# Performance work log

Measured on AMD Instinct MI355X. Metric: run time of the kernel, lower is better.

## Reference

```python
import jax, jax.numpy as jnp
import numpy as np

D_MODEL = 1024
NUM_HEADS = 16
HEAD_DIM = D_MODEL // NUM_HEADS


def setup_inputs() -> dict:
    key = jax.random.key(0)
    ks = jax.random.split(key, 5)
    B, S, D_IN = 2, 2048, 1024
    x = jax.random.normal(ks[0], (B, S, D_IN), dtype=jnp.float32)
    std = 0.02
    wq = jax.random.normal(ks[1], (D_MODEL, D_IN), dtype=jnp.float32) * std
    wk = jax.random.normal(ks[2], (D_MODEL, D_IN), dtype=jnp.float32) * std
    wv = jax.random.normal(ks[3], (D_MODEL, D_IN), dtype=jnp.float32) * std
    wo = jax.random.normal(ks[4], (D_IN, D_MODEL), dtype=jnp.float32) * std
    return {"x": x, "wq": wq, "wk": wk, "wv": wv, "wo": wo}


def _mha(x, wq, wk, wv, wo):
    B, S, _ = x.shape
    H, Dh = NUM_HEADS, HEAD_DIM
    # projections: Linear applies x @ W.T with W of shape [out, in]
    q = (x @ wq.T).reshape(B, S, H, Dh).transpose(0, 2, 1, 3)  # [B,H,S,Dh]
    k = (x @ wk.T).reshape(B, S, H, Dh).transpose(0, 2, 1, 3)
    v = (x @ wv.T).reshape(B, S, H, Dh).transpose(0, 2, 1, 3)
    scores = jnp.einsum('bhqd,bhkd->bhqk', q, k) / jnp.sqrt(jnp.float32(Dh))
    causal = jnp.tril(jnp.ones((S, S), dtype=bool))  # True where attended
    scores = jnp.where(causal, scores, -jnp.inf)
    attn = jax.nn.softmax(scores, axis=-1)
    out = jnp.einsum('bhqk,bhkd->bhqd', attn, v)  # [B,H,S,Dh]
    out = out.transpose(0, 2, 1, 3).reshape(B, S, H * Dh)
    return out @ wo.T


def reference(x, wq, wk, wv, wo):
    return _mha(x, wq, wk, wv, wo)
```

## Files before the change

### kernel.cpp

```cpp
#include <hip/hip_runtime.h>
#include <hip/hip_bf16.h>
#include <stdint.h>

using bf16 = __hip_bfloat16;
typedef __attribute__((ext_vector_type(4))) short shorts4;
typedef __attribute__((ext_vector_type(8))) short short8;
typedef __attribute__((ext_vector_type(4))) float floatx4;
typedef __attribute__((ext_vector_type(16))) float floatx16;
typedef __attribute__((ext_vector_type(4))) unsigned int uintx4;

constexpr int BATCH = 2;
constexpr int SEQ   = 2048;
constexpr int NH    = 16;
constexpr int DH    = 64;
constexpr int DM    = 1024;
constexpr int MROWS = BATCH * SEQ;
constexpr int OUTN  = MROWS * DM;
constexpr int WN    = DM * DM;

__device__ inline short bfbits(float x) {
    bf16 h = __float2bfloat16(x);
    return __builtin_bit_cast(short, h);
}

__device__ inline unsigned pack2(float a, float b) {
    return (unsigned)(unsigned short)bfbits(a) |
           ((unsigned)(unsigned short)bfbits(b) << 16);
}

__device__ inline void async16(bf16* lds, const bf16* g) {
    __builtin_amdgcn_global_load_lds(
        (const __attribute__((address_space(1))) unsigned int*)g,
        (__attribute__((address_space(3))) unsigned int*)lds, 16, 0, 0);
}

__device__ inline void cvt8(const float* src, bf16* dst) {
    float4 f0 = *(const float4*)(src);
    float4 f1 = *(const float4*)(src + 4);
    short8 o;
    o[0] = bfbits(f0.x); o[1] = bfbits(f0.y); o[2] = bfbits(f0.z); o[3] = bfbits(f0.w);
    o[4] = bfbits(f1.x); o[5] = bfbits(f1.y); o[6] = bfbits(f1.z); o[7] = bfbits(f1.w);
    *(short8*)(dst) = o;
}

__global__ __launch_bounds__(256)
void cvt_all(const float* __restrict__ x,  const float* __restrict__ wq,
             const float* __restrict__ wk, const float* __restrict__ wv,
             const float* __restrict__ wo, bf16* __restrict__ dst,
             bf16* __restrict__ wob)
{
    const size_t i = ((size_t)blockIdx.x * 256 + threadIdx.x) * 8;
    if (i < (size_t)OUTN + 3 * WN) {
        const float* src; size_t off;
        if (i < (size_t)OUTN)               { src = x;  off = i; }
        else if (i < (size_t)OUTN + WN)     { src = wq; off = i - OUTN; }
        else if (i < (size_t)OUTN + 2 * WN) { src = wk; off = i - OUTN - WN; }
        else                                { src = wv; off = i - OUTN - 2 * (size_t)WN; }
        cvt8(src + off, dst + i);
    } else {
        const size_t off = i - OUTN - 3 * (size_t)WN;
        cvt8(wo + off, wob + off);
    }
}

__global__ __launch_bounds__(256)
void cvt_inputs(const float* __restrict__ x,  const float* __restrict__ wq,
                const float* __restrict__ wk, const float* __restrict__ wv,
                bf16* __restrict__ dst)
{
    const size_t i = ((size_t)blockIdx.x * 256 + threadIdx.x) * 8;
    const float* src; size_t off;
    if (i < (size_t)OUTN)               { src = x;  off = i; }
    else if (i < (size_t)OUTN + WN)     { src = wq; off = i - OUTN; }
    else if (i < (size_t)OUTN + 2 * WN) { src = wk; off = i - OUTN - WN; }
    else                                { src = wv; off = i - OUTN - 2 * (size_t)WN; }
    cvt8(src + off, dst + i);
}

__global__ __launch_bounds__(256)
void cvt_wo(const float* __restrict__ wo, bf16* __restrict__ dst)
{
    const size_t i = ((size_t)blockIdx.x * 256 + threadIdx.x) * 8;
    cvt8(wo + i, dst + i);
}

template<int MODE, int NZ>
__global__ __launch_bounds__(512, 2)
void gemm_mfma(const bf16* __restrict__ A,
               const bf16* __restrict__ W0, const bf16* __restrict__ W1,
               const bf16* __restrict__ W2,
               bf16* __restrict__ C0, bf16* __restrict__ C1, bf16* __restrict__ C2,
               float* __restrict__ F)
{
    __shared__ __align__(16) bf16 smem[(1 + NZ) * 8192 * 2];

    const int t    = threadIdx.x;
    const int wave = t >> 6;
    const int lane = t & 63;
    const int quad = lane >> 4;
    const int l16  = lane & 15;
    const int m0 = blockIdx.y * 128;
    const int n0 = blockIdx.x * 128;
    const int wr = (wave >> 2) * 64;
    const int wc = (wave & 3) * 32;

    const bf16* Wp[3] = {W0, W1, W2};

    floatx4 acc[NZ][4][2] = {};

    auto stage = [&](int kt, int bb) {
        bf16* Bb = smem + bb * (1 + NZ) * 8192;
        const int k0 = kt * 64;
        #pragma unroll
        for (int p = 0; p < 2; p++) {
            const int ck = p * 512 + t;
            const int kr = ck >> 3;
            const int kg = (ck & 7) ^ (kr & 7);
            async16(Bb + ck * 8, A + (size_t)(m0 + kr) * DM + k0 + kg * 8);
            #pragma unroll
            for (int zz = 0; zz < NZ; zz++)
                async16(Bb + (1 + zz) * 8192 + ck * 8,
                        Wp[zz] + (size_t)(n0 + kr) * DM + k0 + kg * 8);
        }
    };

    stage(0, 0);
    __syncthreads();

    for (int kt = 0; kt < DM / 64; ++kt) {
        const int cur = kt & 1;
        if (kt + 1 < DM / 64) stage(kt + 1, cur ^ 1);

        const bf16* Bb = smem + cur * (1 + NZ) * 8192;

        #pragma unroll
        for (int ks = 0; ks < 2; ks++) {
            short8 af[4];
            #pragma unroll
            for (int i = 0; i < 4; i++) {
                const int r = wr + i * 16 + l16;
                af[i] = *(const short8*)(Bb + r * 64 + ((ks * 4 + quad) ^ (r & 7)) * 8);
            }
            #pragma unroll
            for (int zz = 0; zz < NZ; zz++) {
                short8 wf[2];
                #pragma unroll
                for (int j = 0; j < 2; j++) {
                    const int n = wc + j * 16 + l16;
                    wf[j] = *(const short8*)(Bb + (1 + zz) * 8192 + n * 64 +
                                             ((ks * 4 + quad) ^ (n & 7)) * 8);
                }
                __builtin_amdgcn_s_setprio(1);
                #pragma unroll
                for (int i = 0; i < 4; i++)
                    #pragma unroll
                    for (int j = 0; j < 2; j++)
                        acc[zz][i][j] = __builtin_amdgcn_mfma_f32_16x16x32_bf16(
                            af[i], wf[j], acc[zz][i][j], 0, 0, 0);
                __builtin_amdgcn_s_setprio(0);
            }
        }
        __syncthreads();
    }

    #pragma unroll
    for (int zz = 0; zz < NZ; zz++) {
        #pragma unroll
        for (int i = 0; i < 4; i++) {
            #pragma unroll
            for (int j = 0; j < 2; j++) {
                if (MODE == 0 && zz == 2) {
                    const int s0 = m0 + wr + i * 16 + quad * 4;
                    const int gn = n0 + wc + j * 16 + l16;
                    const int b = s0 >> 11, sr = s0 & (SEQ - 1);
                    const int h = gn >> 6,  d = gn & (DH - 1);
                    shorts4 pv;
                    #pragma unroll
                    for (int r = 0; r < 4; r++) pv[r] = bfbits(acc[zz][i][j][r]);
                    *(shorts4*)(C2 + (((size_t)(b * NH + h)) * DH + d) * SEQ + sr) = pv;
                } else {
                    #pragma unroll
                    for (int r = 0; r < 4; r++) {
                        const int gm = m0 + wr + i * 16 + quad * 4 + r;
                        const int gn = n0 + wc + j * 16 + l16;
                        if (MODE == 1) {
                            F[(size_t)gm * DM + gn] = acc[zz][i][j][r];
                        } else {
                            float av = acc[zz][i][j][r];
                            if (zz == 0) av *= 0.18033688f;
                            bf16* dst = (zz == 0) ? C0 : C1;
                            dst[(size_t)gm * DM + gn] = __float2bfloat16(av);
                        }
                    }
                }
            }
        }
    }
}

__global__ __launch_bounds__(512, 4)
void attn_flash(bf16* __restrict__ Q, const bf16* __restrict__ K,
                const bf16* __restrict__ Vt)
{
    __shared__ __align__(16) bf16 smem[32768];

    const int t    = threadIdx.x;
    const int wave = t >> 6;
    const int lane = t & 63;
    const int hi   = lane >> 5;
    const int l32  = lane & 31;

    const int h  = blockIdx.y;
    const int b  = blockIdx.z;
    const int qt = (blockIdx.x + 5 * h + 8 * b) & 15;
    const int q0 = qt * 128;
    const int hc = h * DH;
    const size_t rowb = (size_t)b * SEQ;
    const size_t bhv  = ((size_t)(b * NH + h)) * SEQ * DH;

    const int qw    = wave & 3;
    const int khalf = wave >> 2;
    const int qrow  = q0 + qw * 32;
    const int qg    = qrow + l32;

    short8 qf[4];
    #pragma unroll
    for (int s = 0; s < 4; s++)
        qf[s] = *(const short8*)(Q + (rowb + qg) * DM + hc + s * 16 + hi * 8);

    floatx16 oacc[2] = {};
    float lsum = 0.f;

    const int T = q0 / 128 + 1;

    auto stage = [&](int tt, int bb) {
        bf16* Kb = smem + bb * 16384;
        bf16* Vb = Kb + 8192;
        const int k0 = tt * 128;
        #pragma unroll
        for (int p = 0; p < 2; p++) {
            const int ck = p * 512 + t;
            const int kr = ck >> 3;
            const int kg = (ck & 7) ^ (kr & 7);
            async16(Kb + ck * 8, K + (rowb + k0 + kr) * DM + hc + kg * 8);
            const int vr = ck >> 4;
            const int vg = (ck & 15) ^ (vr & 15);
            async16(Vb + ck * 8, Vt + bhv + (size_t)vr * SEQ + k0 + vg * 8);
        }
    };

    stage(0, 0);
    __syncthreads();

    for (int tt = 0; tt < T; ++tt) {
        const int cur = tt & 1;
        if (tt + 1 < T) stage(tt + 1, cur ^ 1);

        const bf16* Ks = smem + cur * 16384;
        const bf16* Vs = Ks + 8192;
        const int kbase = tt * 128 + khalf * 64;

        if (kbase <= qrow + 31) {
            #pragma unroll
            for (int kt = 0; kt < 2; kt++) {
                const int kb = kbase + kt * 32;
                if (kb > qrow + 31) continue;

                const int krow = khalf * 64 + kt * 32 + l32;
                floatx16 sc = {};
                #pragma unroll
                for (int s = 0; s < 4; s++) {
                    const int g = (s * 2 + hi) ^ (krow & 7);
                    short8 kf = *(const short8*)(Ks + krow * 64 + g * 8);
                    sc = __builtin_amdgcn_mfma_f32_32x32x16_bf16(kf, qf[s], sc, 0, 0, 0);
                }

                if (kb + 31 > qrow) {
                    #pragma unroll
                    for (int r = 0; r < 16; r++) {
                        const int key = kb + (r & 3) + 8 * (r >> 2) + 4 * hi;
                        sc[r] = (key <= qg) ? sc[r] : -1e30f;
                    }
                }

                #pragma unroll
                for (int r = 0; r < 16; r++) {
                    const float p = __builtin_amdgcn_exp2f(sc[r]);
                    sc[r] = p;
                    lsum += p;
                }

                unsigned d[4][2];
                #pragma unroll
                for (int g = 0; g < 4; g++) {
                    d[g][0] = pack2(sc[4 * g + 0], sc[4 * g + 1]);
                    d[g][1] = pack2(sc[4 * g + 2], sc[4 * g + 3]);
                }

                #pragma unroll
                for (int h16 = 0; h16 < 2; h16++) {
                    const unsigned a0 = d[h16 * 2][0],     a1 = d[h16 * 2][1];
                    const unsigned b0 = d[h16 * 2 + 1][0], b1 = d[h16 * 2 + 1][1];
                    const unsigned mine0 = hi ? b0 : a0, mine1 = hi ? b1 : a1;
                    const unsigned give0 = hi ? a0 : b0, give1 = hi ? a1 : b1;
                    const unsigned r0 = (unsigned)__shfl_xor((int)give0, 32, 64);
                    const unsigned r1 = (unsigned)__shfl_xor((int)give1, 32, 64);
                    uintx4 pw;
                    pw[0] = hi ? r0 : mine0;
                    pw[1] = hi ? r1 : mine1;
                    pw[2] = hi ? mine0 : r0;
                    pw[3] = hi ? mine1 : r1;
                    short8 pb = __builtin_bit_cast(short8, pw);

                    const int Gbase = khalf * 8 + kt * 4 + h16 * 2 + hi;
                    #pragma unroll
                    for (int tile = 0; tile < 2; tile++) {
                        const int vrow = tile * 32 + l32;
                        const int vg = Gbase ^ (vrow & 15);
                        short8 vf = *(const short8*)(Vs + vrow * 128 + vg * 8);
                        oacc[tile] = __builtin_amdgcn_mfma_f32_32x32x16_bf16(vf, pb, oacc[tile], 0, 0, 0);
                    }
                }
            }
        }
        __syncthreads();
    }

    lsum += __shfl_xor(lsum, 32, 64);

    float* dmp = (float*)smem;
    float* lP  = dmp + 4 * 32 * 65;
    if (wave >= 4) {
        const int p = wave - 4;
        #pragma unroll
        for (int tile = 0; tile < 2; tile++)
            #pragma unroll
            for (int r = 0; r < 16; r++) {
                const int d = tile * 32 + (r & 3) + 8 * (r >> 2) + 4 * hi;
                dmp[(p * 32 + l32) * 65 + d] = oacc[tile][r];
            }
        if (!hi) lP[p * 32 + l32] = lsum;
    }
    __syncthreads();

    if (wave < 4) {
        const int p = wave;
        lsum += lP[p * 32 + l32];
        const float invl = 1.0f / lsum;

        bf16* T8 = smem + 16896 + wave * (32 * 72);
        #pragma unroll
        for (int tile = 0; tile < 2; tile++)
            #pragma unroll
            for (int rq = 0; rq < 4; rq++) {
                shorts4 v4;
                #pragma unroll
                for (int s = 0; s < 4; s++) {
                    const int r = rq * 4 + s;
                    const int d = tile * 32 + (r & 3) + 8 * (r >> 2) + 4 * hi;
                    const float comb = oacc[tile][r] + dmp[(p * 32 + l32) * 65 + d];
                    v4[s] = bfbits(comb * invl);
                }
                *(shorts4*)(T8 + l32 * 72 + tile * 32 + rq * 8 + hi * 4) = v4;
            }
        asm volatile("s_waitcnt lgkmcnt(0)" ::: "memory");
        #pragma unroll
        for (int p2 = 0; p2 < 4; p2++) {
            const int rq = (lane >> 3) + p2 * 8;
            const int dd = (lane & 7) * 8;
            short8 v8 = *(const short8*)(T8 + rq * 72 + dd);
            *(short8*)(Q + (rowb + qrow + rq) * DM + hc + dd) = v8;
        }
    }
}

extern "C" void kernel_launch(void* const* d_in, const int* in_sizes, int n_in,
                              void* d_out, int out_size, void* d_ws, size_t ws_size,
                              hipStream_t stream)
{
    const float* x  = (const float*)d_in[0];
    const float* wq = (const float*)d_in[1];
    const float* wk = (const float*)d_in[2];
    const float* wv = (const float*)d_in[3];
    const float* wo = (const float*)d_in[4];
    float* out = (float*)d_out;

    bf16* qb = (bf16*)d_ws;
    bf16* kb = qb + (size_t)OUTN;
    bf16* vb = kb + (size_t)OUTN;

    bf16* xb  = (bf16*)d_out;
    bf16* wqb = xb + (size_t)OUTN;
    bf16* wkb = wqb + WN;
    bf16* wvb = wkb + WN;

    const bool wsBig = ws_size >= (size_t)(3 * (size_t)OUTN + WN) * sizeof(bf16);

    if (wsBig) {
        bf16* wob = vb + (size_t)OUTN;
        cvt_all<<<(OUTN + 4 * WN) / (8 * 256), 256, 0, stream>>>(
            x, wq, wk, wv, wo, xb, wob);
        gemm_mfma<0, 3><<<dim3(DM / 128, MROWS / 128), dim3(512), 0, stream>>>(
            xb, wqb, wkb, wvb, qb, kb, vb, nullptr);
        attn_flash<<<dim3(SEQ / 128, NH, BATCH), dim3(512), 0, stream>>>(qb, kb, vb);
        gemm_mfma<1, 1><<<dim3(DM / 128, MROWS / 128), dim3(512), 0, stream>>>(
            qb, wob, nullptr, nullptr, nullptr, nullptr, nullptr, out);
    } else {
        cvt_inputs<<<(OUTN + 3 * WN) / (8 * 256), 256, 0, stream>>>(x, wq, wk, wv, xb);
        gemm_mfma<0, 3><<<dim3(DM / 128, MROWS / 128), dim3(512), 0, stream>>>(
            xb, wqb, wkb, wvb, qb, kb, vb, nullptr);
        attn_flash<<<dim3(SEQ / 128, NH, BATCH), dim3(512), 0, stream>>>(qb, kb, vb);
        bf16* wob = kb;
        cvt_wo<<<WN / (8 * 256), 256, 0, stream>>>(wo, wob);
        gemm_mfma<1, 1><<<dim3(DM / 128, MROWS / 128), dim3(512), 0, stream>>>(
            qb, wob, nullptr, nullptr, nullptr, nullptr, nullptr, out);
    }
}
```

Before: 161.3 us.

## Pair complementary causal query tiles per block with triple-buffered K/V pipeline

Each attention block now handles two query tiles, qt and 15-qt, so every block processes the same 17 key tiles and the causal workload is balanced across blocks. The grid is halved. K/V staging moves from a double buffer to a triple buffer with explicit vmcnt waits and raw barriers, so loads run two stages ahead. In exchange, register pressure rises from holding two sets of Q fragments and accumulators, and LDS per block grows, with launch bounds lowered from 4 to 2 to match.

```diff
diff --git a/kernel.cpp b/kernel.cpp
--- a/kernel.cpp
+++ b/kernel.cpp
@@ -198,11 +198,11 @@
     }
 }
 
-__global__ __launch_bounds__(512, 4)
+__global__ __launch_bounds__(512, 2)
 void attn_flash(bf16* __restrict__ Q, const bf16* __restrict__ K,
                 const bf16* __restrict__ Vt)
 {
-    __shared__ __align__(16) bf16 smem[32768];
+    __shared__ __align__(16) bf16 smem[49152];
 
     const int t    = threadIdx.x;
     const int wave = t >> 6;
@@ -210,33 +210,37 @@
     const int hi   = lane >> 5;
     const int l32  = lane & 31;
 
-    const int h  = blockIdx.y;
-    const int b  = blockIdx.z;
-    const int qt = (blockIdx.x + 5 * h + 8 * b) & 15;
-    const int q0 = qt * 128;
-    const int hc = h * DH;
+    const int h   = blockIdx.y;
+    const int b   = blockIdx.z;
+    const int qtA = blockIdx.x;
+    const int qtB = 15 - qtA;
+    const int hc  = h * DH;
     const size_t rowb = (size_t)b * SEQ;
     const size_t bhv  = ((size_t)(b * NH + h)) * SEQ * DH;
 
     const int qw    = wave & 3;
     const int khalf = wave >> 2;
-    const int qrow  = q0 + qw * 32;
-    const int qg    = qrow + l32;
-
-    short8 qf[4];
+    const int qrA = qtA * 128 + qw * 32;
+    const int qrB = qtB * 128 + qw * 32;
+
+    short8 qfA[4], qfB[4];
     #pragma unroll
-    for (int s = 0; s < 4; s++)
-        qf[s] = *(const short8*)(Q + (rowb + qg) * DM + hc + s * 16 + hi * 8);
-
-    floatx16 oacc[2] = {};
-    float lsum = 0.f;
-
-    const int T = q0 / 128 + 1;
-
-    auto stage = [&](int tt, int bb) {
-        bf16* Kb = smem + bb * 16384;
+    for (int sg = 0; sg < 4; sg++) {
+        qfA[sg] = *(const short8*)(Q + (rowb + qrA + l32) * DM + hc + sg * 16 + hi * 8);
+        qfB[sg] = *(const short8*)(Q + (rowb + qrB + l32) * DM + hc + sg * 16 + hi * 8);
+    }
+
+    floatx16 oaccA[2] = {}, oaccB[2] = {};
+    float lsumA = 0.f, lsumB = 0.f;
+
+    constexpr int NSLOT = 17;
+
+    auto slotK0 = [&](int s) { return (s <= qtA ? s : s - qtA - 1) * 128; };
+
+    auto stage = [&](int s) {
+        bf16* Kb = smem + (s % 3) * 16384;
         bf16* Vb = Kb + 8192;
-        const int k0 = tt * 128;
+        const int k0 = slotK0(s);
         #pragma unroll
         for (int p = 0; p < 2; p++) {
             const int ck = p * 512 + t;
@@ -249,127 +253,143 @@
         }
     };
 
-    stage(0, 0);
+    auto computeStage = [&](int s, int k0, int qrow, const short8* qf,
+                            floatx16* oacc, float& lsum) {
+        const int kbase = k0 + khalf * 64;
+        if (kbase > qrow + 31) return;
+        const bf16* Ks = smem + (s % 3) * 16384;
+        const bf16* Vs = Ks + 8192;
+        const int qg = qrow + l32;
+
+        #pragma unroll
+        for (int kt = 0; kt < 2; kt++) {
+            const int kb = kbase + kt * 32;
+            if (kb > qrow + 31) continue;
+
+            const int krow = khalf * 64 + kt * 32 + l32;
+            floatx16 sc = {};
+            #pragma unroll
+            for (int sg = 0; sg < 4; sg++) {
+                const int g = (sg * 2 + hi) ^ (krow & 7);
+                short8 kf = *(const short8*)(Ks + krow * 64 + g * 8);
+                sc = __builtin_amdgcn_mfma_f32_32x32x16_bf16(kf, qf[sg], sc, 0, 0, 0);
+            }
+
+            if (kb + 31 > qrow) {
+                #pragma unroll
+                for (int r = 0; r < 16; r++) {
+                    const int key = kb + (r & 3) + 8 * (r >> 2) + 4 * hi;
+                    sc[r] = (key <= qg) ? sc[r] : -1e30f;
+                }
+            }
+
+            #pragma unroll
+            for (int r = 0; r < 16; r++) {
+                const float p = __builtin_amdgcn_exp2f(sc[r]);
+                sc[r] = p;
+                lsum += p;
+            }
+
+            unsigned d[4][2];
+            #pragma unroll
+            for (int g = 0; g < 4; g++) {
+                d[g][0] = pack2(sc[4 * g + 0], sc[4 * g + 1]);
+                d[g][1] = pack2(sc[4 * g + 2], sc[4 * g + 3]);
+            }
+
+            #pragma unroll
+            for (int h16 = 0; h16 < 2; h16++) {
+                const unsigned a0 = d[h16 * 2][0],     a1 = d[h16 * 2][1];
+                const unsigned b0 = d[h16 * 2 + 1][0], b1 = d[h16 * 2 + 1][1];
+                const unsigned mine0 = hi ? b0 : a0, mine1 = hi ? b1 : a1;
+                const unsigned give0 = hi ? a0 : b0, give1 = hi ? a1 : b1;
+                const unsigned r0 = (unsigned)__shfl_xor((int)give0, 32, 64);
+                const unsigned r1 = (unsigned)__shfl_xor((int)give1, 32, 64);
+                uintx4 pw;
+                pw[0] = hi ? r0 : mine0;
+                pw[1] = hi ? r1 : mine1;
+                pw[2] = hi ? mine0 : r0;
+                pw[3] = hi ? mine1 : r1;
+                short8 pb = __builtin_bit_cast(short8, pw);
+
+                const int Gbase = khalf * 8 + kt * 4 + h16 * 2 + hi;
+                #pragma unroll
+                for (int tile = 0; tile < 2; tile++) {
+                    const int vrow = tile * 32 + l32;
+                    const int vg = Gbase ^ (vrow & 15);
+                    short8 vf = *(const short8*)(Vs + vrow * 128 + vg * 8);
+                    oacc[tile] = __builtin_amdgcn_mfma_f32_32x32x16_bf16(vf, pb, oacc[tile], 0, 0, 0);
+                }
+            }
+        }
+    };
+
+    stage(0);
+    stage(1);
+    for (int s = 0; s < NSLOT - 1; ++s) {
+        asm volatile("s_waitcnt vmcnt(4)" ::: "memory");
+        __builtin_amdgcn_s_barrier();
+        if (s + 2 < NSLOT) stage(s + 2);
+        if (s <= qtA) computeStage(s, s * 128, qrA, qfA, oaccA, lsumA);
+        else          computeStage(s, (s - qtA - 1) * 128, qrB, qfB, oaccB, lsumB);
+    }
+    asm volatile("s_waitcnt vmcnt(0)" ::: "memory");
+    __builtin_amdgcn_s_barrier();
+    computeStage(NSLOT - 1, (NSLOT - 1 - qtA - 1) * 128, qrB, qfB, oaccB, lsumB);
+
+    lsumA += __shfl_xor(lsumA, 32, 64);
+    lsumB += __shfl_xor(lsumB, 32, 64);
+
     __syncthreads();
-
-    for (int tt = 0; tt < T; ++tt) {
-        const int cur = tt & 1;
-        if (tt + 1 < T) stage(tt + 1, cur ^ 1);
-
-        const bf16* Ks = smem + cur * 16384;
-        const bf16* Vs = Ks + 8192;
-        const int kbase = tt * 128 + khalf * 64;
-
-        if (kbase <= qrow + 31) {
-            #pragma unroll
-            for (int kt = 0; kt < 2; kt++) {
-                const int kb = kbase + kt * 32;
-                if (kb > qrow + 31) continue;
-
-                const int krow = khalf * 64 + kt * 32 + l32;
-                floatx16 sc = {};
-                #pragma unroll
-                for (int s = 0; s < 4; s++) {
-                    const int g = (s * 2 + hi) ^ (krow & 7);
-                    short8 kf = *(const short8*)(Ks + krow * 64 + g * 8);
-                    sc = __builtin_amdgcn_mfma_f32_32x32x16_bf16(kf, qf[s], sc, 0, 0, 0);
-                }
-
-                if (kb + 31 > qrow) {
+    float* dmp = (float*)smem;
+    float* lP  = dmp + 2 * 4 * 32 * 66;
+    if (khalf == 1) {
+        #pragma unroll
+        for (int m = 0; m < 2; m++) {
+            const floatx16* oc = m ? oaccB : oaccA;
+            #pragma unroll
+            for (int tile = 0; tile < 2; tile++)
+                #pragma unroll
+                for (int r = 0; r < 16; r++) {
+                    const int dd = tile * 32 + (r & 3) + 8 * (r >> 2) + 4 * hi;
+                    dmp[((m * 4 + qw) * 32 + l32) * 66 + dd] = oc[tile][r];
+                }
+            if (!hi) lP[(m * 4 + qw) * 32 + l32] = m ? lsumB : lsumA;
+        }
+    }
+    __syncthreads();
+
+    if (khalf == 0) {
+        bf16* T8 = smem + 34304 + qw * 2304;
+        #pragma unroll
+        for (int m = 0; m < 2; m++) {
+            const floatx16* oc = m ? oaccB : oaccA;
+            const float lt = (m ? lsumB : lsumA) + lP[(m * 4 + qw) * 32 + l32];
+            const float invl = 1.0f / lt;
+            const int qrow = m ? qrB : qrA;
+            #pragma unroll
+            for (int tile = 0; tile < 2; tile++)
+                #pragma unroll
+                for (int rq = 0; rq < 4; rq++) {
+                    shorts4 v4;
                     #pragma unroll
-                    for (int r = 0; r < 16; r++) {
-                        const int key = kb + (r & 3) + 8 * (r >> 2) + 4 * hi;
-                        sc[r] = (key <= qg) ? sc[r] : -1e30f;
+                    for (int sg = 0; sg < 4; sg++) {
+                        const int r = rq * 4 + sg;
+                        const int dd = tile * 32 + (r & 3) + 8 * (r >> 2) + 4 * hi;
+                        const float comb = oc[tile][r] + dmp[((m * 4 + qw) * 32 + l32) * 66 + dd];
+                        v4[sg] = bfbits(comb * invl);
                     }
-                }
-
-                #pragma unroll
-                for (int r = 0; r < 16; r++) {
-                    const float p = __builtin_amdgcn_exp2f(sc[r]);
-                    sc[r] = p;
-                    lsum += p;
-                }
-
-                unsigned d[4][2];
-                #pragma unroll
-                for (int g = 0; g < 4; g++) {
-                    d[g][0] = pack2(sc[4 * g + 0], sc[4 * g + 1]);
-                    d[g][1] = pack2(sc[4 * g + 2], sc[4 * g + 3]);
-                }
-
-                #pragma unroll
-                for (int h16 = 0; h16 < 2; h16++) {
-                    const unsigned a0 = d[h16 * 2][0],     a1 = d[h16 * 2][1];
-                    const unsigned b0 = d[h16 * 2 + 1][0], b1 = d[h16 * 2 + 1][1];
-                    const unsigned mine0 = hi ? b0 : a0, mine1 = hi ? b1 : a1;
-                    const unsigned give0 = hi ? a0 : b0, give1 = hi ? a1 : b1;
-                    const unsigned r0 = (unsigned)__shfl_xor((int)give0, 32, 64);
-                    const unsigned r1 = (unsigned)__shfl_xor((int)give1, 32, 64);
-                    uintx4 pw;
-                    pw[0] = hi ? r0 : mine0;
-                    pw[1] = hi ? r1 : mine1;
-                    pw[2] = hi ? mine0 : r0;
-                    pw[3] = hi ? mine1 : r1;
-                    short8 pb = __builtin_bit_cast(short8, pw);
-
-                    const int Gbase = khalf * 8 + kt * 4 + h16 * 2 + hi;
-                    #pragma unroll
-                    for (int tile = 0; tile < 2; tile++) {
-                        const int vrow = tile * 32 + l32;
-                        const int vg = Gbase ^ (vrow & 15);
-                        short8 vf = *(const short8*)(Vs + vrow * 128 + vg * 8);
-                        oacc[tile] = __builtin_amdgcn_mfma_f32_32x32x16_bf16(vf, pb, oacc[tile], 0, 0, 0);
-                    }
-                }
-            }
-        }
-        __syncthreads();
-    }
-
-    lsum += __shfl_xor(lsum, 32, 64);
-
-    float* dmp = (float*)smem;
-    float* lP  = dmp + 4 * 32 * 65;
-    if (wave >= 4) {
-        const int p = wave - 4;
-        #pragma unroll
-        for (int tile = 0; tile < 2; tile++)
-            #pragma unroll
-            for (int r = 0; r < 16; r++) {
-                const int d = tile * 32 + (r & 3) + 8 * (r >> 2) + 4 * hi;
-                dmp[(p * 32 + l32) * 65 + d] = oacc[tile][r];
-            }
-        if (!hi) lP[p * 32 + l32] = lsum;
-    }
-    __syncthreads();
-
-    if (wave < 4) {
-        const int p = wave;
-        lsum += lP[p * 32 + l32];
-        const float invl = 1.0f / lsum;
-
-        bf16* T8 = smem + 16896 + wave * (32 * 72);
-        #pragma unroll
-        for (int tile = 0; tile < 2; tile++)
-            #pragma unroll
-            for (int rq = 0; rq < 4; rq++) {
-                shorts4 v4;
-                #pragma unroll
-                for (int s = 0; s < 4; s++) {
-                    const int r = rq * 4 + s;
-                    const int d = tile * 32 + (r & 3) + 8 * (r >> 2) + 4 * hi;
-                    const float comb = oacc[tile][r] + dmp[(p * 32 + l32) * 65 + d];
-                    v4[s] = bfbits(comb * invl);
-                }
-                *(shorts4*)(T8 + l32 * 72 + tile * 32 + rq * 8 + hi * 4) = v4;
-            }
-        asm volatile("s_waitcnt lgkmcnt(0)" ::: "memory");
-        #pragma unroll
-        for (int p2 = 0; p2 < 4; p2++) {
-            const int rq = (lane >> 3) + p2 * 8;
-            const int dd = (lane & 7) * 8;
-            short8 v8 = *(const short8*)(T8 + rq * 72 + dd);
-            *(short8*)(Q + (rowb + qrow + rq) * DM + hc + dd) = v8;
+                    *(shorts4*)(T8 + l32 * 72 + tile * 32 + rq * 8 + hi * 4) = v4;
+                }
+            asm volatile("s_waitcnt lgkmcnt(0)" ::: "memory");
+            #pragma unroll
+            for (int p2 = 0; p2 < 4; p2++) {
+                const int rq = (lane >> 3) + p2 * 8;
+                const int dd = (lane & 7) * 8;
+                short8 v8 = *(const short8*)(T8 + rq * 72 + dd);
+                *(short8*)(Q + (rowb + qrow + rq) * DM + hc + dd) = v8;
+            }
+            asm volatile("s_waitcnt lgkmcnt(0)" ::: "memory");
         }
     }
 }
@@ -402,14 +422,14 @@
             x, wq, wk, wv, wo, xb, wob);
         gemm_mfma<0, 3><<<dim3(DM / 128, MROWS / 128), dim3(512), 0, stream>>>(
             xb, wqb, wkb, wvb, qb, kb, vb, nullptr);
-        attn_flash<<<dim3(SEQ / 128, NH, BATCH), dim3(512), 0, stream>>>(qb, kb, vb);
+        attn_flash<<<dim3(8, NH, BATCH), dim3(512), 0, stream>>>(qb, kb, vb);
         gemm_mfma<1, 1><<<dim3(DM / 128, MROWS / 128), dim3(512), 0, stream>>>(
             qb, wob, nullptr, nullptr, nullptr, nullptr, nullptr, out);
     } else {
         cvt_inputs<<<(OUTN + 3 * WN) / (8 * 256), 256, 0, stream>>>(x, wq, wk, wv, xb);
         gemm_mfma<0, 3><<<dim3(DM / 128, MROWS / 128), dim3(512), 0, stream>>>(
             xb, wqb, wkb, wvb, qb, kb, vb, nullptr);
-        attn_flash<<<dim3(SEQ / 128, NH, BATCH), dim3(512), 0, stream>>>(qb, kb, vb);
+        attn_flash<<<dim3(8, NH, BATCH), dim3(512), 0, stream>>>(qb, kb, vb);
         bf16* wob = kb;
         cvt_wo<<<WN / (8 * 256), 256, 0, stream>>>(wo, wob);
         gemm_mfma<1, 1><<<dim3(DM / 128, MROWS / 128), dim3(512), 0, stream>>>(
```

Result: no change. 159.1 us (-1.4%).
